# Kernel optimization log

Measured on AMD Instinct MI355X. Metric: run time of the kernel, lower is better.

Reference implementation:

```python
import jax, jax.numpy as jnp
import numpy as np

TEMPERATURE = 1.0

def _rope_cos_sin(T, D):
    # inv_freq over even indices 0..D step 2 -> D//2 freqs
    inv_freq = 1.0 / (10000.0 ** (jnp.arange(0, D, 2, dtype=jnp.float32) / D))
    t = jnp.arange(T, dtype=jnp.float32)
    freqs = jnp.einsum('i,j->ij', t, inv_freq)          # [T, D//2]
    emb = jnp.concatenate([freqs, freqs], axis=-1)      # [T, D]
    return jnp.cos(emb), jnp.sin(emb)                   # each [T, D]

def _apply_rope(x, cos, sin):
    # x: [B,H,T,D]; cos/sin: [T,D] broadcast over B,H
    D = x.shape[-1]
    half = D // 2
    x1, x2 = x[..., :half], x[..., half:2 * half]
    c = cos[None, None, :, :half]
    s = sin[None, None, :, :half]
    rot = jnp.concatenate([x1 * c - x2 * s, x1 * s + x2 * c], axis=-1)
    if D > 2 * half:
        rot = jnp.concatenate([rot, x[..., 2 * half:]], axis=-1)
    return rot

def setup_inputs() -> dict:
    key = jax.random.key(0)
    kq, kk, kv = jax.random.split(key, 3)
    B, H, T, D = 2, 16, 2048, 64
    return {
        'q': jax.random.normal(kq, (B, H, T, D), dtype=jnp.float32),
        'k': jax.random.normal(kk, (B, H, T, D), dtype=jnp.float32),
        'v': jax.random.normal(kv, (B, H, T, D), dtype=jnp.float32),
    }

def reference(q, k, v):
    B, H, T, D = q.shape
    cos, sin = _rope_cos_sin(T, D)
    qr = _apply_rope(q, cos, sin)
    kr = _apply_rope(k, cos, sin)
    scale = jnp.sqrt(jnp.float32(D)) * TEMPERATURE
    scores = jnp.einsum('bhtd,bhsd->bhts', qr, kr) / scale  # [B,H,T,T]
    # original subtracts row max then softmax; identical to stable softmax
    attn = jax.nn.softmax(scores, axis=-1)
    out = jnp.einsum('bhts,bhsd->bhtd', attn, v)
    return out, attn
```

## Files before the change

kernel.cpp:

```cpp
#include <hip/hip_runtime.h>
#include <hip/hip_bf16.h>
#include <math.h>


#define T_SEQ  2048
#define D_HEAD 64
#define BH_N   32
#define NCH    32
#define OUT_ELEMS (BH_N * T_SEQ * D_HEAD)

typedef __attribute__((ext_vector_type(8))) short bf16x8;
typedef __attribute__((ext_vector_type(4))) float f32x4;

__device__ __forceinline__ unsigned short f2bf(float x) {
    __hip_bfloat16 h = __float2bfloat16(x);
    return *reinterpret_cast<unsigned short*>(&h);
}

__device__ __forceinline__ int swz(int o) { return o ^ (((o >> 7) & 7) << 4); }
__device__ __forceinline__ int tswz(int row, int bcol) {
    return row * 256 + (bcol ^ ((row & 7) << 4));
}

__global__ void rope_table_kernel(float* __restrict__ ctab, float* __restrict__ stab) {
    int i = blockIdx.x * blockDim.x + threadIdx.x;
    if (i >= T_SEQ * 32) return;
    int t = i >> 5;
    int j = i & 31;
    float invf = powf(10000.0f, -(float)j / 32.0f);
    float a = (float)t * invf;
    ctab[i] = cosf(a);
    stab[i] = sinf(a);
}

__global__ __launch_bounds__(256)
void ropebf16_kernel(const float* __restrict__ Q, const float* __restrict__ K,
                     const float* __restrict__ ctab, const float* __restrict__ stab,
                     unsigned short* __restrict__ Qb, unsigned short* __restrict__ Kb,
                     float qscale)
{
    const int r  = blockIdx.x * 16 + (threadIdx.x >> 4);
    const int c4 = threadIdx.x & 15;
    const int t  = r & (T_SEQ - 1);
    const float* X = blockIdx.y ? K : Q;
    unsigned short* H = blockIdx.y ? Kb : Qb;
    const float scale = blockIdx.y ? 1.0f : qscale;
    const float4* xr = (const float4*)(X + (size_t)r * 64);
    float4 a = xr[c4];
    float4 b = xr[c4 ^ 8];
    float4 c = ((const float4*)(ctab + t * 32))[c4 & 7];
    float4 s = ((const float4*)(stab + t * 32))[c4 & 7];
    float4 ro;
    if (c4 < 8) {
        ro.x = a.x * c.x - b.x * s.x; ro.y = a.y * c.y - b.y * s.y;
        ro.z = a.z * c.z - b.z * s.z; ro.w = a.w * c.w - b.w * s.w;
    } else {
        ro.x = a.x * c.x + b.x * s.x; ro.y = a.y * c.y + b.y * s.y;
        ro.z = a.z * c.z + b.z * s.z; ro.w = a.w * c.w + b.w * s.w;
    }
    ushort4 h;
    h.x = f2bf(ro.x * scale); h.y = f2bf(ro.y * scale);
    h.z = f2bf(ro.z * scale); h.w = f2bf(ro.w * scale);
    *(ushort4*)(H + (size_t)r * 64 + c4 * 4) = h;
}

__global__ __launch_bounds__(256)
void vtbf16_kernel(const float* __restrict__ V, unsigned short* __restrict__ Vt)
{
    __shared__ float tile[64][65];
    const int bh = blockIdx.y;
    const int tt = blockIdx.x;
    const float* vg = V + ((size_t)bh * T_SEQ + tt * 64) * 64;
    #pragma unroll
    for (int i = 0; i < 4; ++i) {
        const int row = (threadIdx.x >> 4) + i * 16;
        const int c4  = threadIdx.x & 15;
        float4 a = *(const float4*)(vg + (size_t)row * 64 + c4 * 4);
        tile[row][c4 * 4 + 0] = a.x; tile[row][c4 * 4 + 1] = a.y;
        tile[row][c4 * 4 + 2] = a.z; tile[row][c4 * 4 + 3] = a.w;
    }
    __syncthreads();
    #pragma unroll
    for (int i = 0; i < 4; ++i) {
        const int d   = (threadIdx.x >> 4) + i * 16;
        const int tc4 = threadIdx.x & 15;
        ushort4 h;
        h.x = f2bf(tile[tc4 * 4 + 0][d]);
        h.y = f2bf(tile[tc4 * 4 + 1][d]);
        h.z = f2bf(tile[tc4 * 4 + 2][d]);
        h.w = f2bf(tile[tc4 * 4 + 3][d]);
        *(ushort4*)(Vt + ((size_t)bh * 64 + d) * T_SEQ + tt * 64 + tc4 * 4) = h;
    }
}

__global__ __launch_bounds__(256, 4)
void attn_mfma_kernel(const unsigned short* __restrict__ Qb,
                      const unsigned short* __restrict__ Kb,
                      const unsigned short* __restrict__ Vt,
                      float* __restrict__ out, float* __restrict__ attn)
{
    __shared__ __align__(16) unsigned short kbuf[3][64][64];
    __shared__ __align__(16) float tbuf[4][16 * 64];

    const int tid  = threadIdx.x;
    const int lane = tid & 63;
    const int w    = tid >> 6;
    const int lrow = lane & 15;
    const int lgrp = lane >> 4;

    const int lid = blockIdx.x;
    const int vid = (lid & 7) * 128 + (lid >> 3);
    const int bh  = vid >> 5;
    const int m   = vid & 31;
    const int t0  = m * 64 + w * 16;

    const size_t base = (size_t)bh * T_SEQ * D_HEAD;
    const char* kgb = (const char*)(Kb + base);
    const unsigned short* vgb = Vt + (size_t)bh * 64 * T_SEQ;

    bf16x8 qf0, qf1;
    {
        const unsigned short* qp = Qb + base + (size_t)(t0 + lrow) * 64 + lgrp * 8;
        qf0 = *(const bf16x8*)(qp);
        qf1 = *(const bf16x8*)(qp + 32);
    }

    const int so0 = w * 1024 + lane * 16;
    const int so1 = so0 + 4096;
    const int sq0 = swz(so0);
    const int sq1 = swz(so1);
    char* klds = (char*)&kbuf[0][0][0];
    char* tlds = (char*)&tbuf[w][0];

#define STAGE_K(b, cc) do { \
    __builtin_amdgcn_global_load_lds((const unsigned int*)(kgb + (size_t)(cc) * 8192 + sq0), \
        (unsigned int*)(klds + (b) * 8192 + w * 1024), 16, 0, 0); \
    __builtin_amdgcn_global_load_lds((const unsigned int*)(kgb + (size_t)(cc) * 8192 + sq1), \
        (unsigned int*)(klds + (b) * 8192 + 4096 + w * 1024), 16, 0, 0); \
} while (0)

    float rpa0 = 0.f, rpa1 = 0.f, rpa2 = 0.f, rpa3 = 0.f;
    STAGE_K(0, 0);
    STAGE_K(1, 1);
    for (int cc = 0; cc < NCH; ++cc) {
        if (cc < NCH - 1) { asm volatile("s_waitcnt vmcnt(2)" ::: "memory"); }
        else              { asm volatile("s_waitcnt vmcnt(0)" ::: "memory"); }
        __builtin_amdgcn_s_barrier();
        if (cc + 2 < NCH) STAGE_K((cc + 2) % 3, cc + 2);
        __builtin_amdgcn_sched_barrier(0);
        const char* kb = klds + (cc % 3) * 8192;
        #pragma unroll
        for (int nt = 0; nt < 4; ++nt) {
            const int o = (nt * 16 + lrow) * 128 + lgrp * 16;
            bf16x8 a0 = *(const bf16x8*)(kb + swz(o));
            bf16x8 a1 = *(const bf16x8*)(kb + swz(o + 64));
            f32x4 acc = (f32x4){0.f, 0.f, 0.f, 0.f};
            acc = __builtin_amdgcn_mfma_f32_16x16x32_bf16(a0, qf0, acc, 0, 0, 0);
            acc = __builtin_amdgcn_mfma_f32_16x16x32_bf16(a1, qf1, acc, 0, 0, 0);
            rpa0 += __builtin_amdgcn_exp2f(acc[0]);
            rpa1 += __builtin_amdgcn_exp2f(acc[1]);
            rpa2 += __builtin_amdgcn_exp2f(acc[2]);
            rpa3 += __builtin_amdgcn_exp2f(acc[3]);
        }
    }
    float rp = (rpa0 + rpa1) + (rpa2 + rpa3);
    rp += __shfl_xor(rp, 16, 64);
    rp += __shfl_xor(rp, 32, 64);
    const float inv = 1.0f / rp;

    __builtin_amdgcn_sched_barrier(0);
    __builtin_amdgcn_s_barrier();

    f32x4 o4[4];
    #pragma unroll
    for (int nd = 0; nd < 4; ++nd) o4[nd] = (f32x4){0.f, 0.f, 0.f, 0.f};

    float* abase = attn + (size_t)bh * T_SEQ * T_SEQ;

    STAGE_K(0, 0);
    STAGE_K(1, 1);
    bf16x8 vf[8];
    #pragma unroll
    for (int nd = 0; nd < 4; ++nd)
        #pragma unroll
        for (int ks = 0; ks < 2; ++ks)
            vf[nd * 2 + ks] = *(const bf16x8*)(vgb + (size_t)(nd * 16 + lrow) * T_SEQ
                                               + ks * 32 + lgrp * 8);
    asm volatile("s_waitcnt vmcnt(10)" ::: "memory");

    for (int cc = 0; cc < NCH; ++cc) {
        __builtin_amdgcn_s_barrier();
        __builtin_amdgcn_sched_barrier(0);

        const char* kb = klds + (cc % 3) * 8192;
        f32x4 s4[4];
        #pragma unroll
        for (int nt = 0; nt < 4; ++nt) {
            const int o = (nt * 16 + lrow) * 128 + lgrp * 16;
            bf16x8 a0 = *(const bf16x8*)(kb + swz(o));
            bf16x8 a1 = *(const bf16x8*)(kb + swz(o + 64));
            f32x4 acc = (f32x4){0.f, 0.f, 0.f, 0.f};
            acc = __builtin_amdgcn_mfma_f32_16x16x32_bf16(a0, qf0, acc, 0, 0, 0);
            acc = __builtin_amdgcn_mfma_f32_16x16x32_bf16(a1, qf1, acc, 0, 0, 0);
            s4[nt] = acc;
        }
        #pragma unroll
        for (int nt = 0; nt < 4; ++nt) {
            s4[nt][0] = __builtin_amdgcn_exp2f(s4[nt][0]) * inv;
            s4[nt][1] = __builtin_amdgcn_exp2f(s4[nt][1]) * inv;
            s4[nt][2] = __builtin_amdgcn_exp2f(s4[nt][2]) * inv;
            s4[nt][3] = __builtin_amdgcn_exp2f(s4[nt][3]) * inv;
        }
        #pragma unroll
        for (int nt = 0; nt < 4; ++nt)
            *(f32x4*)(tlds + tswz(lrow, (nt * 16 + lgrp * 4) * 4)) = s4[nt];
        asm volatile("s_waitcnt lgkmcnt(0)" ::: "memory");
        __builtin_amdgcn_sched_barrier(0);

        #pragma unroll
        for (int ks = 0; ks < 2; ++ks) {
            f32x4 pa0 = *(const f32x4*)(tlds + tswz(lrow, (ks * 32 + lgrp * 8) * 4));
            f32x4 pa1 = *(const f32x4*)(tlds + tswz(lrow, (ks * 32 + lgrp * 8 + 4) * 4));
            bf16x8 pa;
            pa[0] = (short)f2bf(pa0[0]); pa[1] = (short)f2bf(pa0[1]);
            pa[2] = (short)f2bf(pa0[2]); pa[3] = (short)f2bf(pa0[3]);
            pa[4] = (short)f2bf(pa1[0]); pa[5] = (short)f2bf(pa1[1]);
            pa[6] = (short)f2bf(pa1[2]); pa[7] = (short)f2bf(pa1[3]);
            #pragma unroll
            for (int nd = 0; nd < 4; ++nd)
                o4[nd] = __builtin_amdgcn_mfma_f32_16x16x32_bf16(pa, vf[nd * 2 + ks], o4[nd], 0, 0, 0);
        }
        f32x4 tr[4];
        #pragma unroll
        for (int i = 0; i < 4; ++i)
            tr[i] = *(const f32x4*)(tlds + tswz(i * 4 + (lane >> 4), (lane & 15) * 16));
        __builtin_amdgcn_sched_barrier(0);
        if (cc + 1 < NCH) {
            #pragma unroll
            for (int nd = 0; nd < 4; ++nd)
                #pragma unroll
                for (int ks = 0; ks < 2; ++ks)
                    vf[nd * 2 + ks] = *(const bf16x8*)(vgb + (size_t)(nd * 16 + lrow) * T_SEQ
                                                       + (cc + 1) * 64 + ks * 32 + lgrp * 8);
        }
        if (cc + 2 < NCH) STAGE_K((cc + 2) % 3, cc + 2);
        __builtin_amdgcn_sched_barrier(0);
        #pragma unroll
        for (int i = 0; i < 4; ++i)
            __builtin_nontemporal_store(tr[i],
                (f32x4*)(abase + (size_t)(t0 + i * 4 + (lane >> 4)) * T_SEQ
                         + cc * 64 + (lane & 15) * 4));
        __builtin_amdgcn_sched_barrier(0);
        if (cc < NCH - 2)      { asm volatile("s_waitcnt vmcnt(18)" ::: "memory"); }
        else if (cc < NCH - 1) { asm volatile("s_waitcnt vmcnt(16)" ::: "memory"); }
    }

    #pragma unroll
    for (int nd = 0; nd < 4; ++nd)
        #pragma unroll
        for (int j = 0; j < 4; ++j)
            __builtin_nontemporal_store(o4[nd][j],
                out + base + (size_t)(t0 + lgrp * 4 + j) * D_HEAD + nd * 16 + lrow);

#undef STAGE_K
}

extern "C" void kernel_launch(void* const* d_in, const int* in_sizes, int n_in,
                              void* d_out, int out_size, void* d_ws, size_t ws_size,
                              hipStream_t stream) {
    const float* q = (const float*)d_in[0];
    const float* k = (const float*)d_in[1];
    const float* v = (const float*)d_in[2];
    float* out  = (float*)d_out;
    float* attn = out + (size_t)OUT_ELEMS;

    float* ctab = (float*)d_ws;
    float* stab = ctab + T_SEQ * 32;
    unsigned short* wsu = (unsigned short*)(stab + T_SEQ * 32);
    const size_t NE = (size_t)BH_N * T_SEQ * D_HEAD;
    unsigned short* Qb = wsu + 0 * NE;
    unsigned short* Kb = wsu + 1 * NE;
    unsigned short* Vt = wsu + 2 * NE;

    const float QSCALE = 0.18033688011112042f;

    rope_table_kernel<<<dim3((T_SEQ * 32 + 255) / 256), dim3(256), 0, stream>>>(ctab, stab);
    ropebf16_kernel<<<dim3(BH_N * T_SEQ / 16, 2), dim3(256), 0, stream>>>(q, k, ctab, stab, Qb, Kb, QSCALE);
    vtbf16_kernel<<<dim3(T_SEQ / 64, BH_N), dim3(256), 0, stream>>>(v, Vt);
    attn_mfma_kernel<<<dim3(BH_N * T_SEQ / 64), dim3(256), 0, stream>>>(Qb, Kb, Vt, out, attn);
}
```

Measured before the change: 183.5 us.

## Split softmax denominator pass across waves by key chunks, reduce via LDS

The first pass computing row sums of exp(scores) changes so that each wave handles 8 of the 32 key chunks for all 64 query rows, loading K fragments straight from global memory into registers. Previously every wave iterated over all 32 chunks through a triple-buffered LDS pipeline. Partial sums are reduced across waves through shared memory, which costs two extra barriers. This drops the LDS staging and per-chunk barriers from the first pass, but uses more registers, issues uncoalesced direct global K loads, and leaves a stray no-op statement in the transpose kernel.

```diff
diff --git a/kernel.cpp b/kernel.cpp
--- a/kernel.cpp
+++ b/kernel.cpp
@@ -89,6 +89,7 @@
         h.y = f2bf(tile[tc4 * 4 + 1][d]);
         h.z = f2bf(tile[tc4 * 4 + 2][d]);
         h.w = f2bf(tile[tc4 * 4 + 3][d]);
+        *(unsigned short*)&h;
         *(ushort4*)(Vt + ((size_t)bh * 64 + d) * T_SEQ + tt * 64 + tc4 * 4) = h;
     }
 }
@@ -116,14 +117,58 @@
 
     const size_t base = (size_t)bh * T_SEQ * D_HEAD;
     const char* kgb = (const char*)(Kb + base);
+    const unsigned short* kgs = Kb + base;
     const unsigned short* vgb = Vt + (size_t)bh * 64 * T_SEQ;
 
-    bf16x8 qf0, qf1;
     {
-        const unsigned short* qp = Qb + base + (size_t)(t0 + lrow) * 64 + lgrp * 8;
-        qf0 = *(const bf16x8*)(qp);
-        qf1 = *(const bf16x8*)(qp + 32);
-    }
+        bf16x8 qa[4][2];
+        #pragma unroll
+        for (int rg = 0; rg < 4; ++rg) {
+            const unsigned short* qp = Qb + base + (size_t)(m * 64 + rg * 16 + lrow) * 64 + lgrp * 8;
+            qa[rg][0] = *(const bf16x8*)(qp);
+            qa[rg][1] = *(const bf16x8*)(qp + 32);
+        }
+        float rpa[4] = {0.f, 0.f, 0.f, 0.f};
+        for (int c = 0; c < 8; ++c) {
+            const int cc = w * 8 + c;
+            bf16x8 kf[4][2];
+            #pragma unroll
+            for (int nt = 0; nt < 4; ++nt) {
+                const unsigned short* kp = kgs + (size_t)(cc * 64 + nt * 16 + lrow) * 64 + lgrp * 8;
+                kf[nt][0] = *(const bf16x8*)(kp);
+                kf[nt][1] = *(const bf16x8*)(kp + 32);
+            }
+            #pragma unroll
+            for (int rg = 0; rg < 4; ++rg) {
+                float r0 = 0.f;
+                #pragma unroll
+                for (int nt = 0; nt < 4; ++nt) {
+                    f32x4 acc = (f32x4){0.f, 0.f, 0.f, 0.f};
+                    acc = __builtin_amdgcn_mfma_f32_16x16x32_bf16(kf[nt][0], qa[rg][0], acc, 0, 0, 0);
+                    acc = __builtin_amdgcn_mfma_f32_16x16x32_bf16(kf[nt][1], qa[rg][1], acc, 0, 0, 0);
+                    r0 += __builtin_amdgcn_exp2f(acc[0]) + __builtin_amdgcn_exp2f(acc[1])
+                        + __builtin_amdgcn_exp2f(acc[2]) + __builtin_amdgcn_exp2f(acc[3]);
+                }
+                rpa[rg] += r0;
+            }
+        }
+        #pragma unroll
+        for (int rg = 0; rg < 4; ++rg) {
+            rpa[rg] += __shfl_xor(rpa[rg], 16, 64);
+            rpa[rg] += __shfl_xor(rpa[rg], 32, 64);
+        }
+        if (lane < 16) {
+            #pragma unroll
+            for (int rg = 0; rg < 4; ++rg)
+                tbuf[0][w * 64 + rg * 16 + lrow] = rpa[rg];
+        }
+    }
+    __builtin_amdgcn_sched_barrier(0);
+    __builtin_amdgcn_s_barrier();
+    const float inv = 1.0f / (tbuf[0][0 * 64 + w * 16 + lrow] + tbuf[0][1 * 64 + w * 16 + lrow]
+                            + tbuf[0][2 * 64 + w * 16 + lrow] + tbuf[0][3 * 64 + w * 16 + lrow]);
+    __builtin_amdgcn_sched_barrier(0);
+    __builtin_amdgcn_s_barrier();
 
     const int so0 = w * 1024 + lane * 16;
     const int so1 = so0 + 4096;
@@ -139,37 +184,12 @@
         (unsigned int*)(klds + (b) * 8192 + 4096 + w * 1024), 16, 0, 0); \
 } while (0)
 
-    float rpa0 = 0.f, rpa1 = 0.f, rpa2 = 0.f, rpa3 = 0.f;
-    STAGE_K(0, 0);
-    STAGE_K(1, 1);
-    for (int cc = 0; cc < NCH; ++cc) {
-        if (cc < NCH - 1) { asm volatile("s_waitcnt vmcnt(2)" ::: "memory"); }
-        else              { asm volatile("s_waitcnt vmcnt(0)" ::: "memory"); }
-        __builtin_amdgcn_s_barrier();
-        if (cc + 2 < NCH) STAGE_K((cc + 2) % 3, cc + 2);
-        __builtin_amdgcn_sched_barrier(0);
-        const char* kb = klds + (cc % 3) * 8192;
-        #pragma unroll
-        for (int nt = 0; nt < 4; ++nt) {
-            const int o = (nt * 16 + lrow) * 128 + lgrp * 16;
-            bf16x8 a0 = *(const bf16x8*)(kb + swz(o));
-            bf16x8 a1 = *(const bf16x8*)(kb + swz(o + 64));
-            f32x4 acc = (f32x4){0.f, 0.f, 0.f, 0.f};
-            acc = __builtin_amdgcn_mfma_f32_16x16x32_bf16(a0, qf0, acc, 0, 0, 0);
-            acc = __builtin_amdgcn_mfma_f32_16x16x32_bf16(a1, qf1, acc, 0, 0, 0);
-            rpa0 += __builtin_amdgcn_exp2f(acc[0]);
-            rpa1 += __builtin_amdgcn_exp2f(acc[1]);
-            rpa2 += __builtin_amdgcn_exp2f(acc[2]);
-            rpa3 += __builtin_amdgcn_exp2f(acc[3]);
-        }
-    }
-    float rp = (rpa0 + rpa1) + (rpa2 + rpa3);
-    rp += __shfl_xor(rp, 16, 64);
-    rp += __shfl_xor(rp, 32, 64);
-    const float inv = 1.0f / rp;
-
-    __builtin_amdgcn_sched_barrier(0);
-    __builtin_amdgcn_s_barrier();
+    bf16x8 qf0, qf1;
+    {
+        const unsigned short* qp = Qb + base + (size_t)(t0 + lrow) * 64 + lgrp * 8;
+        qf0 = *(const bf16x8*)(qp);
+        qf1 = *(const bf16x8*)(qp + 32);
+    }
 
     f32x4 o4[4];
     #pragma unroll
```

Result: slower. 196.4 us (+7.0%).
